# Performance work log

Hardware: AMD Instinct MI355X
Metric: run time of the kernel (lower is better)

## Reference

```python
import jax, jax.numpy as jnp
import numpy as np

T, L, D, P, H = 1024, 32, 512, 512, 2048
EPS = 1e-5  # torch LayerNorm default eps


def _layer_norm(x, g, b):
    m = x.mean(axis=-1, keepdims=True)
    v = ((x - m) ** 2).mean(axis=-1, keepdims=True)
    return (x - m) * jax.lax.rsqrt(v + EPS) * g + b


def setup_inputs() -> dict:
    key = jax.random.key(0)
    ks = jax.random.split(key, 16)
    s = 0.02
    inp = {
        "base_prompts": jax.random.normal(ks[0], (T, L, D), jnp.float32),
        "new_prompt": jax.random.normal(ks[1], (L, D), jnp.float32),
        "task_embedding": jax.random.normal(ks[2], (D,), jnp.float32),
        # linear weights stored (in, out) so forward is x @ W + b
        "Wt": jax.random.normal(ks[3], (D, P), jnp.float32) * s,
        "bt": jnp.zeros((P,), jnp.float32),
        "Wq": jax.random.normal(ks[4], (D, P), jnp.float32) * s,
        "bq": jnp.zeros((P,), jnp.float32),
        "Wk": jax.random.normal(ks[5], (D, P), jnp.float32) * s,
        "bk": jnp.zeros((P,), jnp.float32),
        "Wv": jax.random.normal(ks[6], (D, P), jnp.float32) * s,
        "bv": jnp.zeros((P,), jnp.float32),
        "Wo": jax.random.normal(ks[7], (P, D), jnp.float32) * s,
        "bo": jnp.zeros((D,), jnp.float32),
        "Wa1": jax.random.normal(ks[8], (D, H), jnp.float32) * s,
        "ba1": jnp.zeros((H,), jnp.float32),
        "Wa2": jax.random.normal(ks[9], (H, D), jnp.float32) * s,
        "ba2": jnp.zeros((D,), jnp.float32),
        "g_in": jnp.ones((D,), jnp.float32),
        "b_in": jnp.zeros((D,), jnp.float32),
        "g_out": jnp.ones((D,), jnp.float32),
        "b_out": jnp.zeros((D,), jnp.float32),
    }
    return inp


def reference(base_prompts, new_prompt, task_embedding,
              Wt, bt, Wq, bq, Wk, bk, Wv, bv, Wo, bo,
              Wa1, ba1, Wa2, ba2, g_in, b_in, g_out, b_out):
    scale = 1.0 / np.sqrt(P).astype(np.float32)

    # --- task conditioning ---
    task_vec = jnp.tanh(task_embedding @ Wt + bt)                 # [P]
    key_repr = (base_prompts @ Wk + bk).mean(axis=1)              # [T,P]
    scores = (key_repr @ task_vec) * scale                        # [T]
    task_weights = jax.nn.softmax(scores)
    conditioned = base_prompts * (1.0 + task_weights[:, None, None])  # [T,L,D]

    query = new_prompt @ Wq + bq                                  # [L,P]
    keys = conditioned @ Wk + bk                                  # [T,L,P]
    values = conditioned @ Wv + bv                                # [T,L,P]

    # --- task-level attention ---
    pooled_q = query.mean(axis=0)                                 # [P]
    pooled_k = keys.mean(axis=1)                                  # [T,P]
    task_attn = jax.nn.softmax((pooled_k @ pooled_q) * scale)     # [T]
    task_weights = 0.5 * task_weights + 0.5 * task_attn
    task_weights = task_weights / jnp.maximum(task_weights.sum(), 1e-6)

    # --- enhanced mode: weighted pooling over tasks ---
    weighted_values = jnp.einsum('t,tlp->lp', task_weights, values)       # [L,P]
    weighted_keys = jnp.einsum('t,tlp->lp', task_weights, keys)           # [L,P]
    weighted_prompts = jnp.einsum('t,tld->ld', task_weights, conditioned) # [L,D]

    # --- feature-level attention ---
    feature_logits = (query @ weighted_keys.T) * scale            # [L,L]
    feature_attn = jax.nn.softmax(feature_logits, axis=-1)
    evolved_proj = feature_attn @ weighted_values                 # [L,P]

    evolved = evolved_proj @ Wo + bo                              # [L,D]
    evolved = _layer_norm(weighted_prompts + evolved, g_in, b_in)
    mlp = jax.nn.relu(evolved @ Wa1 + ba1) @ Wa2 + ba2
    aligned = _layer_norm(evolved + mlp, g_out, b_out)            # [L,D]

    aligned_prompts = jnp.broadcast_to(aligned, (T, L, D))        # stack of identical aligned prompts
    return aligned, aligned_prompts, task_weights, feature_attn
```

## Files before the change

### kernel.cpp

```cpp
#include <hip/hip_runtime.h>


typedef unsigned int u32;

static constexpr int T_ = 1024, L_ = 32, D_ = 512, P_ = 512, H_ = 2048;
static constexpr float SCALE = 0.04419417382415922f;
static constexpr float EPS_ = 1e-5f;

static constexpr int OFF_QUERY   = 0;
static constexpr int OFF_TV      = 16384;
static constexpr int OFF_PQ      = 16896;
static constexpr int OFF_WKTV    = 17408;
static constexpr int OFF_WKPQ    = 17920;
static constexpr int OFF_U       = 18432;
static constexpr int OFF_V       = 19456;
static constexpr int OFF_C       = 20480;
static constexpr int OFF_PART    = 21504;
static constexpr int OFF_WBASE   = 545792;
static constexpr int OFF_WKEY    = 562176;
static constexpr int OFF_WVAL    = 578560;
static constexpr int OFF_FA      = 594944;
static constexpr int OFF_EP      = 595968;
static constexpr int OFF_EVOLVED = 612352;
static constexpr int OFF_AQ      = 628736;
static constexpr int OFF_AKV     = 645632;
static constexpr int OFF_AEVO    = 678400;
static constexpr int OFF_AH1     = 694784;
static constexpr int OFF_AOUT    = 760320;
static constexpr int ZERO_BEGIN  = OFF_AQ;
static constexpr int ZERO_F4     = (776704 - 628736) / 4;

static constexpr int OFFO_AL = 0;
static constexpr int OFFO_AP = 16384;
static constexpr int OFFO_TW = 16384 + 16777216;
static constexpr int OFFO_FA = OFFO_TW + 1024;

__device__ __forceinline__ float wred(float v) {
    #pragma unroll
    for (int off = 32; off > 0; off >>= 1) v += __shfl_down(v, off, 64);
    return v;
}
template <int NT>
__device__ __forceinline__ float fsum(float v, float* buf, int tid) {
    v = wred(v);
    if ((tid & 63) == 0) buf[tid >> 6] = v;
    __syncthreads();
    if (tid == 0) { float s = 0.f; for (int i = 0; i < NT / 64; ++i) s += buf[i]; buf[0] = s; }
    __syncthreads();
    float r = buf[0]; __syncthreads();
    return r;
}
template <int NT>
__device__ __forceinline__ float fmaxr(float v, float* buf, int tid) {
    #pragma unroll
    for (int off = 32; off > 0; off >>= 1) v = fmaxf(v, __shfl_down(v, off, 64));
    if ((tid & 63) == 0) buf[tid >> 6] = v;
    __syncthreads();
    if (tid == 0) { float s = buf[0]; for (int i = 1; i < NT / 64; ++i) s = fmaxf(s, buf[i]); buf[0] = s; }
    __syncthreads();
    float r = buf[0]; __syncthreads();
    return r;
}

__global__ void k_zero(float* __restrict__ ws) {
    int i = blockIdx.x * 256 + threadIdx.x;
    if (i < ZERO_F4) ((float4*)(ws + ZERO_BEGIN))[i] = make_float4(0.f, 0.f, 0.f, 0.f);
}

__global__ void k_query_g(const float* __restrict__ np, const float* __restrict__ te,
                          const float* __restrict__ Wq, const float* __restrict__ Wt,
                          float* __restrict__ ws) {
    __shared__ float sx[128];
    int p = threadIdx.x, b = blockIdx.x, kc = blockIdx.y;
    const float* x = (b < L_) ? (np + b * D_) : te;
    if (p < 128) sx[p] = x[kc * 128 + p];
    __syncthreads();
    const float* W = (b < L_) ? Wq : Wt;
    float acc = 0.f;
    #pragma unroll 8
    for (int j = 0; j < 128; ++j) acc = fmaf(sx[j], W[(kc * 128 + j) * P_ + p], acc);
    atomicAdd(&ws[OFF_AQ + b * P_ + p], acc);
}

__global__ void k_query_ep(const float* __restrict__ bq, const float* __restrict__ bt,
                           float* __restrict__ ws) {
    int p = threadIdx.x, b = blockIdx.x;
    if (b < L_) ws[OFF_QUERY + b * P_ + p] = ws[OFF_AQ + b * P_ + p] + bq[p];
    else        ws[OFF_TV + p] = tanhf(ws[OFF_AQ + L_ * P_ + p] + bt[p]);
}

__global__ void k_pq(float* __restrict__ ws) {
    int p = threadIdx.x;
    float s = 0.f;
    for (int l = 0; l < L_; ++l) s += ws[OFF_QUERY + l * P_ + p];
    ws[OFF_PQ + p] = s * (1.0f / L_);
}

__global__ void k_wk2(const float* __restrict__ Wk, float* __restrict__ ws) {
    int tid = threadIdx.x, wv = tid >> 6, lane = tid & 63;
    int d = blockIdx.x * 8 + wv;
    const float4* row = (const float4*)(Wk + d * P_);
    const float4* tv4 = (const float4*)(ws + OFF_TV);
    const float4* pq4 = (const float4*)(ws + OFF_PQ);
    float4 a = row[lane * 2], b = row[lane * 2 + 1];
    float4 t0 = tv4[lane * 2], t1 = tv4[lane * 2 + 1];
    float4 q0 = pq4[lane * 2], q1 = pq4[lane * 2 + 1];
    float pa = a.x * t0.x + a.y * t0.y + a.z * t0.z + a.w * t0.w
             + b.x * t1.x + b.y * t1.y + b.z * t1.z + b.w * t1.w;
    float pb = a.x * q0.x + a.y * q0.y + a.z * q0.z + a.w * q0.w
             + b.x * q1.x + b.y * q1.y + b.z * q1.z + b.w * q1.w;
    pa = wred(pa); pb = wred(pb);
    if (lane == 0) { ws[OFF_WKTV + d] = pa; ws[OFF_WKPQ + d] = pb; }
}

__global__ void k_bbar(const float* __restrict__ base, float* __restrict__ ws) {
    __shared__ float buf[8];
    int t = blockIdx.x, d = threadIdx.x;
    const float* bp = base + (size_t)t * (L_ * D_);
    float s = 0.f;
    for (int l = 0; l < L_; ++l) s += bp[l * D_ + d];
    float up = fsum<512>(s * ws[OFF_WKTV + d], buf, d);
    float vp = fsum<512>(s * ws[OFF_WKPQ + d], buf, d);
    if (d == 0) {
        ws[OFF_U + t] = up * (1.0f / L_);
        ws[OFF_V + t] = vp * (1.0f / L_);
    }
}

__global__ void k_soft(const float* __restrict__ bk, float* __restrict__ out_tw,
                       float* __restrict__ ws) {
    __shared__ float buf[8];
    int tid = threadIdx.x;
    float pbt = 0.f, pbq = 0.f;
    for (int p = tid; p < P_; p += 256) {
        float bkf = bk[p];
        pbt = fmaf(bkf, ws[OFF_TV + p], pbt);
        pbq = fmaf(bkf, ws[OFF_PQ + p], pbq);
    }
    float bkt = fsum<256>(pbt, buf, tid);
    float bkq = fsum<256>(pbq, buf, tid);

    float s1[4], e1[4], tw1[4], lmax = -1e30f;
    #pragma unroll
    for (int k = 0; k < 4; ++k) {
        s1[k] = (ws[OFF_U + tid + k * 256] + bkt) * SCALE;
        lmax = fmaxf(lmax, s1[k]);
    }
    float gmax = fmaxr<256>(lmax, buf, tid);
    float ls = 0.f;
    #pragma unroll
    for (int k = 0; k < 4; ++k) { e1[k] = expf(s1[k] - gmax); ls += e1[k]; }
    float gs = fsum<256>(ls, buf, tid);
    #pragma unroll
    for (int k = 0; k < 4; ++k) tw1[k] = e1[k] / gs;

    float p2[4], e2[4];
    lmax = -1e30f;
    #pragma unroll
    for (int k = 0; k < 4; ++k) {
        p2[k] = ((1.0f + tw1[k]) * ws[OFF_V + tid + k * 256] + bkq) * SCALE;
        lmax = fmaxf(lmax, p2[k]);
    }
    gmax = fmaxr<256>(lmax, buf, tid);
    ls = 0.f;
    #pragma unroll
    for (int k = 0; k < 4; ++k) { e2[k] = expf(p2[k] - gmax); ls += e2[k]; }
    gs = fsum<256>(ls, buf, tid);

    float tw[4], lsum = 0.f;
    #pragma unroll
    for (int k = 0; k < 4; ++k) { tw[k] = 0.5f * tw1[k] + 0.5f * (e2[k] / gs); lsum += tw[k]; }
    float S = fsum<256>(lsum, buf, tid);
    S = fmaxf(S, 1e-6f);
    #pragma unroll
    for (int k = 0; k < 4; ++k) {
        int t = tid + k * 256;
        float twn = tw[k] / S;
        out_tw[t] = twn;
        ws[OFF_C + t] = twn * (1.0f + tw1[k]);
    }
}

__global__ void k_wpart(const float* __restrict__ base, float* __restrict__ ws) {
    __shared__ float cs[32];
    int l = blockIdx.x, ch = blockIdx.y, tid = threadIdx.x;
    if (tid < 32) cs[tid] = ws[OFF_C + ch * 32 + tid];
    __syncthreads();
    float a0 = 0.f, a1 = 0.f, a2 = 0.f, a3 = 0.f;
    for (int i = 0; i < 32; ++i) {
        int t = ch * 32 + i;
        float4 v = ((const float4*)(base + ((size_t)t * L_ + l) * D_))[tid];
        float cc = cs[i];
        a0 = fmaf(cc, v.x, a0); a1 = fmaf(cc, v.y, a1);
        a2 = fmaf(cc, v.z, a2); a3 = fmaf(cc, v.w, a3);
    }
    ((float4*)(ws + OFF_PART + (ch * L_ + l) * D_))[tid] = make_float4(a0, a1, a2, a3);
}

__global__ void k_wred(float* __restrict__ ws) {
    int l = blockIdx.x, d = threadIdx.x;
    float s = 0.f;
    for (int ch = 0; ch < 32; ++ch) s += ws[OFF_PART + (ch * L_ + l) * D_ + d];
    ws[OFF_WBASE + l * D_ + d] = s;
}

__global__ void k_wkv_g(const float* __restrict__ Wk, const float* __restrict__ Wv,
                        float* __restrict__ ws) {
    __shared__ float sx[128];
    int p = threadIdx.x, l = blockIdx.x, sel = blockIdx.y, kc = blockIdx.z;
    if (p < 128) sx[p] = ws[OFF_WBASE + l * D_ + kc * 128 + p];
    __syncthreads();
    const float* W = sel ? Wv : Wk;
    float acc = 0.f;
    #pragma unroll 8
    for (int j = 0; j < 128; ++j) acc = fmaf(sx[j], W[(kc * 128 + j) * P_ + p], acc);
    atomicAdd(&ws[OFF_AKV + (sel * L_ + l) * P_ + p], acc);
}

__global__ void k_wkv_ep(const float* __restrict__ bk, const float* __restrict__ bv,
                         float* __restrict__ ws) {
    int p = threadIdx.x, l = blockIdx.x, sel = blockIdx.y;
    float b = sel ? bv[p] : bk[p];
    ws[(sel ? OFF_WVAL : OFF_WKEY) + l * P_ + p] = ws[OFF_AKV + (sel * L_ + l) * P_ + p] + b;
}

__global__ void k_logits(float* __restrict__ out_fa, float* __restrict__ ws) {
    __shared__ __align__(16) float sq[512];
    __shared__ float lg[32];
    int l = blockIdx.x, tid = threadIdx.x, wv = tid >> 6, lane = tid & 63;
    sq[tid] = ws[OFF_QUERY + l * P_ + tid];
    __syncthreads();
    const float4* sq4 = (const float4*)sq;
    float4 q0 = sq4[lane * 2], q1 = sq4[lane * 2 + 1];
    for (int g = wv * 4; g < wv * 4 + 4; ++g) {
        const float4* kr = (const float4*)(ws + OFF_WKEY + g * P_);
        float4 a = kr[lane * 2], b = kr[lane * 2 + 1];
        float s = a.x * q0.x + a.y * q0.y + a.z * q0.z + a.w * q0.w
                + b.x * q1.x + b.y * q1.y + b.z * q1.z + b.w * q1.w;
        s = wred(s);
        if (lane == 0) lg[g] = s * SCALE;
    }
    __syncthreads();
    if (tid < 32) {
        float mx = -1e30f;
        for (int i = 0; i < 32; ++i) mx = fmaxf(mx, lg[i]);
        float S = 0.f;
        for (int i = 0; i < 32; ++i) S += expf(lg[i] - mx);
        float f = expf(lg[tid] - mx) / S;
        ws[OFF_FA + l * 32 + tid] = f;
        out_fa[l * 32 + tid] = f;
    }
}

__global__ void k_ep(float* __restrict__ ws) {
    __shared__ float fa[32];
    int l = blockIdx.x, p = threadIdx.x;
    if (p < 32) fa[p] = ws[OFF_FA + l * 32 + p];
    __syncthreads();
    float acc = 0.f;
    #pragma unroll 8
    for (int j = 0; j < L_; ++j) acc = fmaf(fa[j], ws[OFF_WVAL + j * P_ + p], acc);
    ws[OFF_EP + l * P_ + p] = acc;
}

__global__ void k_evo_g(const float* __restrict__ Wo, float* __restrict__ ws) {
    __shared__ float sx[128];
    int d = threadIdx.x, l = blockIdx.x, kc = blockIdx.y;
    if (d < 128) sx[d] = ws[OFF_EP + l * P_ + kc * 128 + d];
    __syncthreads();
    float acc = 0.f;
    #pragma unroll 8
    for (int j = 0; j < 128; ++j) acc = fmaf(sx[j], Wo[(kc * 128 + j) * D_ + d], acc);
    atomicAdd(&ws[OFF_AEVO + l * D_ + d], acc);
}

__global__ void k_xin_ln(const float* __restrict__ bo, const float* __restrict__ g_in,
                         const float* __restrict__ b_in, float* __restrict__ ws) {
    __shared__ float buf[8];
    int l = blockIdx.x, d = threadIdx.x;
    float x = ws[OFF_WBASE + l * D_ + d] + ws[OFF_AEVO + l * D_ + d] + bo[d];
    float mean = fsum<512>(x, buf, d) * (1.0f / D_);
    float dx = x - mean;
    float var = fsum<512>(dx * dx, buf, d) * (1.0f / D_);
    ws[OFF_EVOLVED + l * D_ + d] = dx * rsqrtf(var + EPS_) * g_in[d] + b_in[d];
}

__global__ void k_mlp1_g(const float* __restrict__ Wa1, float* __restrict__ ws) {
    __shared__ float sx[128];
    int tid = threadIdx.x, l = blockIdx.x, hc = blockIdx.y, kc = blockIdx.z;
    if (tid < 128) sx[tid] = ws[OFF_EVOLVED + l * D_ + kc * 128 + tid];
    __syncthreads();
    int h = hc * 512 + tid;
    float acc = 0.f;
    #pragma unroll 8
    for (int j = 0; j < 128; ++j) acc = fmaf(sx[j], Wa1[(kc * 128 + j) * H_ + h], acc);
    atomicAdd(&ws[OFF_AH1 + l * H_ + h], acc);
}

__global__ void k_mlp2_g(const float* __restrict__ Wa2, const float* __restrict__ ba1,
                         float* __restrict__ ws) {
    __shared__ float sh[128];
    int d = threadIdx.x, l = blockIdx.x, kc = blockIdx.y;
    if (d < 128) {
        int h = kc * 128 + d;
        sh[d] = fmaxf(ws[OFF_AH1 + l * H_ + h] + ba1[h], 0.f);
    }
    __syncthreads();
    float acc = 0.f;
    #pragma unroll 8
    for (int j = 0; j < 128; ++j) acc = fmaf(sh[j], Wa2[(kc * 128 + j) * D_ + d], acc);
    atomicAdd(&ws[OFF_AOUT + l * D_ + d], acc);
}

__global__ void k_lnout(const float* __restrict__ ba2, const float* __restrict__ g_out,
                        const float* __restrict__ b_out, float* __restrict__ out_al,
                        float* __restrict__ ws) {
    __shared__ float buf[8];
    int l = blockIdx.x, d = threadIdx.x;
    float x = ws[OFF_EVOLVED + l * D_ + d] + ws[OFF_AOUT + l * D_ + d] + ba2[d];
    float mean = fsum<512>(x, buf, d) * (1.0f / D_);
    float dx = x - mean;
    float var = fsum<512>(dx * dx, buf, d) * (1.0f / D_);
    out_al[l * D_ + d] = dx * rsqrtf(var + EPS_) * g_out[d] + b_out[d];
}

__global__ void k_bcast(float* __restrict__ out) {
    const float4* src = (const float4*)out;
    float4* dst = (float4*)(out + OFFO_AP);
    int idx = blockIdx.x * 256 + threadIdx.x;
    #pragma unroll
    for (int k = 0; k < 4; ++k) {
        int v = idx + k * 1048576;
        dst[v] = src[v & 4095];
    }
}

extern "C" void kernel_launch(void* const* d_in, const int* in_sizes, int n_in,
                              void* d_out, int out_size, void* d_ws, size_t ws_size,
                              hipStream_t stream) {
    const float* base = (const float*)d_in[0];
    const float* np   = (const float*)d_in[1];
    const float* te   = (const float*)d_in[2];
    const float* Wt   = (const float*)d_in[3];
    const float* bt   = (const float*)d_in[4];
    const float* Wq   = (const float*)d_in[5];
    const float* bq   = (const float*)d_in[6];
    const float* Wk   = (const float*)d_in[7];
    const float* bk   = (const float*)d_in[8];
    const float* Wv   = (const float*)d_in[9];
    const float* bv   = (const float*)d_in[10];
    const float* Wo   = (const float*)d_in[11];
    const float* bo   = (const float*)d_in[12];
    const float* Wa1  = (const float*)d_in[13];
    const float* ba1  = (const float*)d_in[14];
    const float* Wa2  = (const float*)d_in[15];
    const float* ba2  = (const float*)d_in[16];
    const float* g_in = (const float*)d_in[17];
    const float* b_in = (const float*)d_in[18];
    const float* g_out= (const float*)d_in[19];
    const float* b_out= (const float*)d_in[20];
    float* out = (float*)d_out;
    float* ws = out + OFFO_AP;

    hipLaunchKernelGGL(k_zero,     dim3(145),        dim3(256), 0, stream, ws);
    hipLaunchKernelGGL(k_query_g,  dim3(33, 4),      dim3(512), 0, stream, np, te, Wq, Wt, ws);
    hipLaunchKernelGGL(k_query_ep, dim3(33),         dim3(512), 0, stream, bq, bt, ws);
    hipLaunchKernelGGL(k_pq,       dim3(1),          dim3(512), 0, stream, ws);
    hipLaunchKernelGGL(k_wk2,      dim3(64),         dim3(512), 0, stream, Wk, ws);
    hipLaunchKernelGGL(k_bbar,     dim3(1024),       dim3(512), 0, stream, base, ws);
    hipLaunchKernelGGL(k_soft,     dim3(1),          dim3(256), 0, stream, bk, out + OFFO_TW, ws);
    hipLaunchKernelGGL(k_wpart,    dim3(32, 32),     dim3(128), 0, stream, base, ws);
    hipLaunchKernelGGL(k_wred,     dim3(32),         dim3(512), 0, stream, ws);
    hipLaunchKernelGGL(k_wkv_g,    dim3(32, 2, 4),   dim3(512), 0, stream, Wk, Wv, ws);
    hipLaunchKernelGGL(k_wkv_ep,   dim3(32, 2),      dim3(512), 0, stream, bk, bv, ws);
    hipLaunchKernelGGL(k_logits,   dim3(32),         dim3(512), 0, stream, out + OFFO_FA, ws);
    hipLaunchKernelGGL(k_ep,       dim3(32),         dim3(512), 0, stream, ws);
    hipLaunchKernelGGL(k_evo_g,    dim3(32, 4),      dim3(512), 0, stream, Wo, ws);
    hipLaunchKernelGGL(k_xin_ln,   dim3(32),         dim3(512), 0, stream, bo, g_in, b_in, ws);
    hipLaunchKernelGGL(k_mlp1_g,   dim3(32, 4, 4),   dim3(512), 0, stream, Wa1, ws);
    hipLaunchKernelGGL(k_mlp2_g,   dim3(32, 16),     dim3(512), 0, stream, Wa2, ba1, ws);
    hipLaunchKernelGGL(k_lnout,    dim3(32),         dim3(512), 0, stream, ba2, g_out, b_out, out + OFFO_AL, ws);
    hipLaunchKernelGGL(k_bcast,    dim3(4096),       dim3(256), 0, stream, out);
}
```

Before: 254.6 us.

## Fuse all stages into one cooperative persistent kernel with grid syncs

Replaces the chain of nineteen small kernel launches with a single cooperative kernel of 256 blocks that steps through the stages separated by grid-wide barriers. The L-sum of base_prompts is computed once and stored, and the split-K atomic GEMV stages are replaced by full-K per-block dot products or partial buffers, which removes the zeroing kernel and the atomics. The intent is to cut launch overhead and inter-kernel gaps. In exchange, most stages leave the majority of blocks idle at each barrier, and every grid sync adds its own latency.

Result: slower. 600.6 us (+135.9%).

```diff
diff --git a/kernel.cpp b/kernel.cpp
--- a/kernel.cpp
+++ b/kernel.cpp
@@ -1,4 +1,7 @@
 #include <hip/hip_runtime.h>
+#include <hip/hip_cooperative_groups.h>
+
+namespace cg = cooperative_groups;
 
 
 typedef unsigned int u32;
@@ -15,370 +18,339 @@
 static constexpr int OFF_U       = 18432;
 static constexpr int OFF_V       = 19456;
 static constexpr int OFF_C       = 20480;
-static constexpr int OFF_PART    = 21504;
-static constexpr int OFF_WBASE   = 545792;
-static constexpr int OFF_WKEY    = 562176;
-static constexpr int OFF_WVAL    = 578560;
-static constexpr int OFF_FA      = 594944;
-static constexpr int OFF_EP      = 595968;
-static constexpr int OFF_EVOLVED = 612352;
-static constexpr int OFF_AQ      = 628736;
-static constexpr int OFF_AKV     = 645632;
-static constexpr int OFF_AEVO    = 678400;
-static constexpr int OFF_AH1     = 694784;
-static constexpr int OFF_AOUT    = 760320;
-static constexpr int ZERO_BEGIN  = OFF_AQ;
-static constexpr int ZERO_F4     = (776704 - 628736) / 4;
+static constexpr int OFF_SBUF    = 21504;
+static constexpr int OFF_PART    = 545792;
+static constexpr int OFF_WBASE   = 676864;
+static constexpr int OFF_WKEY    = 693248;
+static constexpr int OFF_WVAL    = 709632;
+static constexpr int OFF_FA      = 726016;
+static constexpr int OFF_EVOLVED = 727040;
+static constexpr int OFF_H1      = 743424;
+static constexpr int OFF_P2      = 808960;
 
 static constexpr int OFFO_AL = 0;
 static constexpr int OFFO_AP = 16384;
 static constexpr int OFFO_TW = 16384 + 16777216;
 static constexpr int OFFO_FA = OFFO_TW + 1024;
 
+struct Params {
+    const float *base, *np, *te, *Wt, *bt, *Wq, *bq, *Wk, *bk, *Wv, *bv,
+                *Wo, *bo, *Wa1, *ba1, *Wa2, *ba2, *g_in, *b_in, *g_out, *b_out;
+    float* out;
+};
+
 __device__ __forceinline__ float wred(float v) {
     #pragma unroll
     for (int off = 32; off > 0; off >>= 1) v += __shfl_down(v, off, 64);
     return v;
 }
-template <int NT>
-__device__ __forceinline__ float fsum(float v, float* buf, int tid) {
+__device__ __forceinline__ float fsum512(float v, float* buf, int tid) {
     v = wred(v);
     if ((tid & 63) == 0) buf[tid >> 6] = v;
     __syncthreads();
-    if (tid == 0) { float s = 0.f; for (int i = 0; i < NT / 64; ++i) s += buf[i]; buf[0] = s; }
-    __syncthreads();
-    float r = buf[0]; __syncthreads();
+    if (tid == 0) { float s = 0.f; for (int i = 0; i < 8; ++i) s += buf[i]; buf[0] = s; }
+    __syncthreads();
+    float r = buf[0];
+    __syncthreads();
     return r;
 }
-template <int NT>
-__device__ __forceinline__ float fmaxr(float v, float* buf, int tid) {
+__device__ __forceinline__ float fmax512(float v, float* buf, int tid) {
     #pragma unroll
     for (int off = 32; off > 0; off >>= 1) v = fmaxf(v, __shfl_down(v, off, 64));
     if ((tid & 63) == 0) buf[tid >> 6] = v;
     __syncthreads();
-    if (tid == 0) { float s = buf[0]; for (int i = 1; i < NT / 64; ++i) s = fmaxf(s, buf[i]); buf[0] = s; }
-    __syncthreads();
-    float r = buf[0]; __syncthreads();
+    if (tid == 0) { float s = buf[0]; for (int i = 1; i < 8; ++i) s = fmaxf(s, buf[i]); buf[0] = s; }
+    __syncthreads();
+    float r = buf[0];
+    __syncthreads();
     return r;
 }
 
-__global__ void k_zero(float* __restrict__ ws) {
-    int i = blockIdx.x * 256 + threadIdx.x;
-    if (i < ZERO_F4) ((float4*)(ws + ZERO_BEGIN))[i] = make_float4(0.f, 0.f, 0.f, 0.f);
-}
-
-__global__ void k_query_g(const float* __restrict__ np, const float* __restrict__ te,
-                          const float* __restrict__ Wq, const float* __restrict__ Wt,
-                          float* __restrict__ ws) {
-    __shared__ float sx[128];
-    int p = threadIdx.x, b = blockIdx.x, kc = blockIdx.y;
-    const float* x = (b < L_) ? (np + b * D_) : te;
-    if (p < 128) sx[p] = x[kc * 128 + p];
-    __syncthreads();
-    const float* W = (b < L_) ? Wq : Wt;
-    float acc = 0.f;
-    #pragma unroll 8
-    for (int j = 0; j < 128; ++j) acc = fmaf(sx[j], W[(kc * 128 + j) * P_ + p], acc);
-    atomicAdd(&ws[OFF_AQ + b * P_ + p], acc);
-}
-
-__global__ void k_query_ep(const float* __restrict__ bq, const float* __restrict__ bt,
-                           float* __restrict__ ws) {
-    int p = threadIdx.x, b = blockIdx.x;
-    if (b < L_) ws[OFF_QUERY + b * P_ + p] = ws[OFF_AQ + b * P_ + p] + bq[p];
-    else        ws[OFF_TV + p] = tanhf(ws[OFF_AQ + L_ * P_ + p] + bt[p]);
-}
-
-__global__ void k_pq(float* __restrict__ ws) {
-    int p = threadIdx.x;
-    float s = 0.f;
-    for (int l = 0; l < L_; ++l) s += ws[OFF_QUERY + l * P_ + p];
-    ws[OFF_PQ + p] = s * (1.0f / L_);
-}
-
-__global__ void k_wk2(const float* __restrict__ Wk, float* __restrict__ ws) {
-    int tid = threadIdx.x, wv = tid >> 6, lane = tid & 63;
-    int d = blockIdx.x * 8 + wv;
-    const float4* row = (const float4*)(Wk + d * P_);
-    const float4* tv4 = (const float4*)(ws + OFF_TV);
-    const float4* pq4 = (const float4*)(ws + OFF_PQ);
-    float4 a = row[lane * 2], b = row[lane * 2 + 1];
-    float4 t0 = tv4[lane * 2], t1 = tv4[lane * 2 + 1];
-    float4 q0 = pq4[lane * 2], q1 = pq4[lane * 2 + 1];
-    float pa = a.x * t0.x + a.y * t0.y + a.z * t0.z + a.w * t0.w
-             + b.x * t1.x + b.y * t1.y + b.z * t1.z + b.w * t1.w;
-    float pb = a.x * q0.x + a.y * q0.y + a.z * q0.z + a.w * q0.w
-             + b.x * q1.x + b.y * q1.y + b.z * q1.z + b.w * q1.w;
-    pa = wred(pa); pb = wred(pb);
-    if (lane == 0) { ws[OFF_WKTV + d] = pa; ws[OFF_WKPQ + d] = pb; }
-}
-
-__global__ void k_bbar(const float* __restrict__ base, float* __restrict__ ws) {
+__global__ void __launch_bounds__(512) k_mega(Params P) {
+    cg::grid_group g = cg::this_grid();
+    __shared__ __align__(16) float sm[576];
     __shared__ float buf[8];
-    int t = blockIdx.x, d = threadIdx.x;
-    const float* bp = base + (size_t)t * (L_ * D_);
-    float s = 0.f;
-    for (int l = 0; l < L_; ++l) s += bp[l * D_ + d];
-    float up = fsum<512>(s * ws[OFF_WKTV + d], buf, d);
-    float vp = fsum<512>(s * ws[OFF_WKPQ + d], buf, d);
-    if (d == 0) {
-        ws[OFF_U + t] = up * (1.0f / L_);
-        ws[OFF_V + t] = vp * (1.0f / L_);
-    }
-}
-
-__global__ void k_soft(const float* __restrict__ bk, float* __restrict__ out_tw,
-                       float* __restrict__ ws) {
-    __shared__ float buf[8];
-    int tid = threadIdx.x;
-    float pbt = 0.f, pbq = 0.f;
-    for (int p = tid; p < P_; p += 256) {
-        float bkf = bk[p];
-        pbt = fmaf(bkf, ws[OFF_TV + p], pbt);
-        pbq = fmaf(bkf, ws[OFF_PQ + p], pbq);
-    }
-    float bkt = fsum<256>(pbt, buf, tid);
-    float bkq = fsum<256>(pbq, buf, tid);
-
-    float s1[4], e1[4], tw1[4], lmax = -1e30f;
-    #pragma unroll
-    for (int k = 0; k < 4; ++k) {
-        s1[k] = (ws[OFF_U + tid + k * 256] + bkt) * SCALE;
-        lmax = fmaxf(lmax, s1[k]);
-    }
-    float gmax = fmaxr<256>(lmax, buf, tid);
-    float ls = 0.f;
-    #pragma unroll
-    for (int k = 0; k < 4; ++k) { e1[k] = expf(s1[k] - gmax); ls += e1[k]; }
-    float gs = fsum<256>(ls, buf, tid);
-    #pragma unroll
-    for (int k = 0; k < 4; ++k) tw1[k] = e1[k] / gs;
-
-    float p2[4], e2[4];
-    lmax = -1e30f;
-    #pragma unroll
-    for (int k = 0; k < 4; ++k) {
-        p2[k] = ((1.0f + tw1[k]) * ws[OFF_V + tid + k * 256] + bkq) * SCALE;
-        lmax = fmaxf(lmax, p2[k]);
-    }
-    gmax = fmaxr<256>(lmax, buf, tid);
-    ls = 0.f;
-    #pragma unroll
-    for (int k = 0; k < 4; ++k) { e2[k] = expf(p2[k] - gmax); ls += e2[k]; }
-    gs = fsum<256>(ls, buf, tid);
-
-    float tw[4], lsum = 0.f;
-    #pragma unroll
-    for (int k = 0; k < 4; ++k) { tw[k] = 0.5f * tw1[k] + 0.5f * (e2[k] / gs); lsum += tw[k]; }
-    float S = fsum<256>(lsum, buf, tid);
-    S = fmaxf(S, 1e-6f);
-    #pragma unroll
-    for (int k = 0; k < 4; ++k) {
-        int t = tid + k * 256;
-        float twn = tw[k] / S;
-        out_tw[t] = twn;
-        ws[OFF_C + t] = twn * (1.0f + tw1[k]);
-    }
-}
-
-__global__ void k_wpart(const float* __restrict__ base, float* __restrict__ ws) {
-    __shared__ float cs[32];
-    int l = blockIdx.x, ch = blockIdx.y, tid = threadIdx.x;
-    if (tid < 32) cs[tid] = ws[OFF_C + ch * 32 + tid];
-    __syncthreads();
-    float a0 = 0.f, a1 = 0.f, a2 = 0.f, a3 = 0.f;
-    for (int i = 0; i < 32; ++i) {
-        int t = ch * 32 + i;
-        float4 v = ((const float4*)(base + ((size_t)t * L_ + l) * D_))[tid];
-        float cc = cs[i];
-        a0 = fmaf(cc, v.x, a0); a1 = fmaf(cc, v.y, a1);
-        a2 = fmaf(cc, v.z, a2); a3 = fmaf(cc, v.w, a3);
-    }
-    ((float4*)(ws + OFF_PART + (ch * L_ + l) * D_))[tid] = make_float4(a0, a1, a2, a3);
-}
-
-__global__ void k_wred(float* __restrict__ ws) {
-    int l = blockIdx.x, d = threadIdx.x;
-    float s = 0.f;
-    for (int ch = 0; ch < 32; ++ch) s += ws[OFF_PART + (ch * L_ + l) * D_ + d];
-    ws[OFF_WBASE + l * D_ + d] = s;
-}
-
-__global__ void k_wkv_g(const float* __restrict__ Wk, const float* __restrict__ Wv,
-                        float* __restrict__ ws) {
-    __shared__ float sx[128];
-    int p = threadIdx.x, l = blockIdx.x, sel = blockIdx.y, kc = blockIdx.z;
-    if (p < 128) sx[p] = ws[OFF_WBASE + l * D_ + kc * 128 + p];
-    __syncthreads();
-    const float* W = sel ? Wv : Wk;
-    float acc = 0.f;
-    #pragma unroll 8
-    for (int j = 0; j < 128; ++j) acc = fmaf(sx[j], W[(kc * 128 + j) * P_ + p], acc);
-    atomicAdd(&ws[OFF_AKV + (sel * L_ + l) * P_ + p], acc);
-}
-
-__global__ void k_wkv_ep(const float* __restrict__ bk, const float* __restrict__ bv,
-                         float* __restrict__ ws) {
-    int p = threadIdx.x, l = blockIdx.x, sel = blockIdx.y;
-    float b = sel ? bv[p] : bk[p];
-    ws[(sel ? OFF_WVAL : OFF_WKEY) + l * P_ + p] = ws[OFF_AKV + (sel * L_ + l) * P_ + p] + b;
-}
-
-__global__ void k_logits(float* __restrict__ out_fa, float* __restrict__ ws) {
-    __shared__ __align__(16) float sq[512];
-    __shared__ float lg[32];
-    int l = blockIdx.x, tid = threadIdx.x, wv = tid >> 6, lane = tid & 63;
-    sq[tid] = ws[OFF_QUERY + l * P_ + tid];
-    __syncthreads();
-    const float4* sq4 = (const float4*)sq;
-    float4 q0 = sq4[lane * 2], q1 = sq4[lane * 2 + 1];
-    for (int g = wv * 4; g < wv * 4 + 4; ++g) {
-        const float4* kr = (const float4*)(ws + OFF_WKEY + g * P_);
-        float4 a = kr[lane * 2], b = kr[lane * 2 + 1];
-        float s = a.x * q0.x + a.y * q0.y + a.z * q0.z + a.w * q0.w
-                + b.x * q1.x + b.y * q1.y + b.z * q1.z + b.w * q1.w;
-        s = wred(s);
-        if (lane == 0) lg[g] = s * SCALE;
-    }
-    __syncthreads();
-    if (tid < 32) {
-        float mx = -1e30f;
-        for (int i = 0; i < 32; ++i) mx = fmaxf(mx, lg[i]);
-        float S = 0.f;
-        for (int i = 0; i < 32; ++i) S += expf(lg[i] - mx);
-        float f = expf(lg[tid] - mx) / S;
-        ws[OFF_FA + l * 32 + tid] = f;
-        out_fa[l * 32 + tid] = f;
-    }
-}
-
-__global__ void k_ep(float* __restrict__ ws) {
-    __shared__ float fa[32];
-    int l = blockIdx.x, p = threadIdx.x;
-    if (p < 32) fa[p] = ws[OFF_FA + l * 32 + p];
-    __syncthreads();
-    float acc = 0.f;
-    #pragma unroll 8
-    for (int j = 0; j < L_; ++j) acc = fmaf(fa[j], ws[OFF_WVAL + j * P_ + p], acc);
-    ws[OFF_EP + l * P_ + p] = acc;
-}
-
-__global__ void k_evo_g(const float* __restrict__ Wo, float* __restrict__ ws) {
-    __shared__ float sx[128];
-    int d = threadIdx.x, l = blockIdx.x, kc = blockIdx.y;
-    if (d < 128) sx[d] = ws[OFF_EP + l * P_ + kc * 128 + d];
-    __syncthreads();
-    float acc = 0.f;
-    #pragma unroll 8
-    for (int j = 0; j < 128; ++j) acc = fmaf(sx[j], Wo[(kc * 128 + j) * D_ + d], acc);
-    atomicAdd(&ws[OFF_AEVO + l * D_ + d], acc);
-}
-
-__global__ void k_xin_ln(const float* __restrict__ bo, const float* __restrict__ g_in,
-                         const float* __restrict__ b_in, float* __restrict__ ws) {
-    __shared__ float buf[8];
-    int l = blockIdx.x, d = threadIdx.x;
-    float x = ws[OFF_WBASE + l * D_ + d] + ws[OFF_AEVO + l * D_ + d] + bo[d];
-    float mean = fsum<512>(x, buf, d) * (1.0f / D_);
-    float dx = x - mean;
-    float var = fsum<512>(dx * dx, buf, d) * (1.0f / D_);
-    ws[OFF_EVOLVED + l * D_ + d] = dx * rsqrtf(var + EPS_) * g_in[d] + b_in[d];
-}
-
-__global__ void k_mlp1_g(const float* __restrict__ Wa1, float* __restrict__ ws) {
-    __shared__ float sx[128];
-    int tid = threadIdx.x, l = blockIdx.x, hc = blockIdx.y, kc = blockIdx.z;
-    if (tid < 128) sx[tid] = ws[OFF_EVOLVED + l * D_ + kc * 128 + tid];
-    __syncthreads();
-    int h = hc * 512 + tid;
-    float acc = 0.f;
-    #pragma unroll 8
-    for (int j = 0; j < 128; ++j) acc = fmaf(sx[j], Wa1[(kc * 128 + j) * H_ + h], acc);
-    atomicAdd(&ws[OFF_AH1 + l * H_ + h], acc);
-}
-
-__global__ void k_mlp2_g(const float* __restrict__ Wa2, const float* __restrict__ ba1,
-                         float* __restrict__ ws) {
-    __shared__ float sh[128];
-    int d = threadIdx.x, l = blockIdx.x, kc = blockIdx.y;
-    if (d < 128) {
-        int h = kc * 128 + d;
-        sh[d] = fmaxf(ws[OFF_AH1 + l * H_ + h] + ba1[h], 0.f);
-    }
-    __syncthreads();
-    float acc = 0.f;
-    #pragma unroll 8
-    for (int j = 0; j < 128; ++j) acc = fmaf(sh[j], Wa2[(kc * 128 + j) * D_ + d], acc);
-    atomicAdd(&ws[OFF_AOUT + l * D_ + d], acc);
-}
-
-__global__ void k_lnout(const float* __restrict__ ba2, const float* __restrict__ g_out,
-                        const float* __restrict__ b_out, float* __restrict__ out_al,
-                        float* __restrict__ ws) {
-    __shared__ float buf[8];
-    int l = blockIdx.x, d = threadIdx.x;
-    float x = ws[OFF_EVOLVED + l * D_ + d] + ws[OFF_AOUT + l * D_ + d] + ba2[d];
-    float mean = fsum<512>(x, buf, d) * (1.0f / D_);
-    float dx = x - mean;
-    float var = fsum<512>(dx * dx, buf, d) * (1.0f / D_);
-    out_al[l * D_ + d] = dx * rsqrtf(var + EPS_) * g_out[d] + b_out[d];
-}
-
-__global__ void k_bcast(float* __restrict__ out) {
-    const float4* src = (const float4*)out;
-    float4* dst = (float4*)(out + OFFO_AP);
-    int idx = blockIdx.x * 256 + threadIdx.x;
-    #pragma unroll
-    for (int k = 0; k < 4; ++k) {
-        int v = idx + k * 1048576;
-        dst[v] = src[v & 4095];
+    const int b = blockIdx.x, tid = threadIdx.x;
+    float* out = P.out;
+    float* ws = out + OFFO_AP;
+
+    for (int i = 0; i < 4; ++i) {
+        int t = b + i * 256;
+        const float* bp = P.base + (size_t)t * (L_ * D_) + tid;
+        float s = 0.f;
+        #pragma unroll
+        for (int l = 0; l < L_; ++l) s += bp[l * D_];
+        ws[OFF_SBUF + t * D_ + tid] = s;
+    }
+    if (b < 33) {
+        const float* x = (b < L_) ? (P.np + b * D_) : P.te;
+        const float* W = (b < L_) ? P.Wq : P.Wt;
+        sm[tid] = x[tid];
+        __syncthreads();
+        float a0 = 0, a1 = 0, a2 = 0, a3 = 0;
+        for (int d = 0; d < D_; d += 4) {
+            a0 = fmaf(sm[d],     W[(size_t)(d)     * P_ + tid], a0);
+            a1 = fmaf(sm[d + 1], W[(size_t)(d + 1) * P_ + tid], a1);
+            a2 = fmaf(sm[d + 2], W[(size_t)(d + 2) * P_ + tid], a2);
+            a3 = fmaf(sm[d + 3], W[(size_t)(d + 3) * P_ + tid], a3);
+        }
+        float acc = (a0 + a1) + (a2 + a3);
+        if (b < L_) ws[OFF_QUERY + b * P_ + tid] = acc + P.bq[tid];
+        else        ws[OFF_TV + tid] = tanhf(acc + P.bt[tid]);
+    }
+    g.sync();
+
+    if (b < 64) {
+        float s = 0.f;
+        #pragma unroll
+        for (int l = 0; l < L_; ++l) s += ws[OFF_QUERY + l * P_ + tid];
+        s *= (1.0f / L_);
+        sm[tid] = s;
+        if (b == 0) ws[OFF_PQ + tid] = s;
+        __syncthreads();
+        int wv = tid >> 6, lane = tid & 63;
+        int d = b * 8 + wv;
+        const float4* row = (const float4*)(P.Wk + (size_t)d * P_);
+        const float4* tv4 = (const float4*)(ws + OFF_TV);
+        const float4* pq4 = (const float4*)sm;
+        float4 a = row[lane * 2], c = row[lane * 2 + 1];
+        float4 t0 = tv4[lane * 2], t1 = tv4[lane * 2 + 1];
+        float4 q0 = pq4[lane * 2], q1 = pq4[lane * 2 + 1];
+        float pa = a.x * t0.x + a.y * t0.y + a.z * t0.z + a.w * t0.w
+                 + c.x * t1.x + c.y * t1.y + c.z * t1.z + c.w * t1.w;
+        float pb = a.x * q0.x + a.y * q0.y + a.z * q0.z + a.w * q0.w
+                 + c.x * q1.x + c.y * q1.y + c.z * q1.z + c.w * q1.w;
+        pa = wred(pa); pb = wred(pb);
+        if (lane == 0) { ws[OFF_WKTV + d] = pa; ws[OFF_WKPQ + d] = pb; }
+    }
+    g.sync();
+
+    {
+        float wt = ws[OFF_WKTV + tid], wq = ws[OFF_WKPQ + tid];
+        for (int i = 0; i < 4; ++i) {
+            int t = b * 4 + i;
+            float s = ws[OFF_SBUF + t * D_ + tid];
+            float up = fsum512(s * wt, buf, tid);
+            float vp = fsum512(s * wq, buf, tid);
+            if (tid == 0) {
+                ws[OFF_U + t] = up * (1.0f / L_);
+                ws[OFF_V + t] = vp * (1.0f / L_);
+            }
+        }
+    }
+    g.sync();
+
+    if (b == 0) {
+        float bkt = fsum512(P.bk[tid] * ws[OFF_TV + tid], buf, tid);
+        float bkq = fsum512(P.bk[tid] * ws[OFF_PQ + tid], buf, tid);
+
+        float s1[2], e1[2], tw1[2], lmax = -1e30f;
+        #pragma unroll
+        for (int k = 0; k < 2; ++k) {
+            s1[k] = (ws[OFF_U + tid + k * 512] + bkt) * SCALE;
+            lmax = fmaxf(lmax, s1[k]);
+        }
+        float gmax = fmax512(lmax, buf, tid);
+        float ls = 0.f;
+        #pragma unroll
+        for (int k = 0; k < 2; ++k) { e1[k] = expf(s1[k] - gmax); ls += e1[k]; }
+        float gs = fsum512(ls, buf, tid);
+        #pragma unroll
+        for (int k = 0; k < 2; ++k) tw1[k] = e1[k] / gs;
+
+        float p2[2], e2[2];
+        lmax = -1e30f;
+        #pragma unroll
+        for (int k = 0; k < 2; ++k) {
+            p2[k] = ((1.0f + tw1[k]) * ws[OFF_V + tid + k * 512] + bkq) * SCALE;
+            lmax = fmaxf(lmax, p2[k]);
+        }
+        gmax = fmax512(lmax, buf, tid);
+        ls = 0.f;
+        #pragma unroll
+        for (int k = 0; k < 2; ++k) { e2[k] = expf(p2[k] - gmax); ls += e2[k]; }
+        gs = fsum512(ls, buf, tid);
+
+        float tw[2], lsum = 0.f;
+        #pragma unroll
+        for (int k = 0; k < 2; ++k) { tw[k] = 0.5f * tw1[k] + 0.5f * (e2[k] / gs); lsum += tw[k]; }
+        float S = fsum512(lsum, buf, tid);
+        S = fmaxf(S, 1e-6f);
+        #pragma unroll
+        for (int k = 0; k < 2; ++k) {
+            int t = tid + k * 512;
+            float twn = tw[k] / S;
+            out[OFFO_TW + t] = twn;
+            ws[OFF_C + t] = twn * (1.0f + tw1[k]);
+        }
+    }
+    g.sync();
+
+    {
+        int l = b >> 3, tc = b & 7;
+        if (tid < 128) sm[tid] = ws[OFF_C + tc * 128 + tid];
+        __syncthreads();
+        const float* bp = P.base + ((size_t)(tc * 128) * L_ + l) * D_ + tid;
+        float acc = 0.f;
+        for (int i = 0; i < 128; ++i)
+            acc = fmaf(sm[i], bp[(size_t)i * (L_ * D_)], acc);
+        ws[OFF_PART + (l * 8 + tc) * D_ + tid] = acc;
+    }
+    g.sync();
+
+    if (b < 64) {
+        int l = b >> 1, sel = b & 1;
+        float wsum = 0.f;
+        #pragma unroll
+        for (int tc = 0; tc < 8; ++tc) wsum += ws[OFF_PART + (l * 8 + tc) * D_ + tid];
+        sm[tid] = wsum;
+        if (sel == 0) ws[OFF_WBASE + l * D_ + tid] = wsum;
+        __syncthreads();
+        const float* W = sel ? P.Wv : P.Wk;
+        float a0 = 0, a1 = 0, a2 = 0, a3 = 0;
+        for (int d = 0; d < D_; d += 4) {
+            a0 = fmaf(sm[d],     W[(size_t)(d)     * P_ + tid], a0);
+            a1 = fmaf(sm[d + 1], W[(size_t)(d + 1) * P_ + tid], a1);
+            a2 = fmaf(sm[d + 2], W[(size_t)(d + 2) * P_ + tid], a2);
+            a3 = fmaf(sm[d + 3], W[(size_t)(d + 3) * P_ + tid], a3);
+        }
+        float acc = (a0 + a1) + (a2 + a3) + (sel ? P.bv[tid] : P.bk[tid]);
+        ws[(sel ? OFF_WVAL : OFF_WKEY) + l * P_ + tid] = acc;
+    }
+    g.sync();
+
+    if (b < 32) {
+        sm[tid] = ws[OFF_QUERY + b * P_ + tid];
+        __syncthreads();
+        int wv = tid >> 6, lane = tid & 63;
+        const float4* sq4 = (const float4*)sm;
+        float4 q0 = sq4[lane * 2], q1 = sq4[lane * 2 + 1];
+        for (int gg = wv * 4; gg < wv * 4 + 4; ++gg) {
+            const float4* kr = (const float4*)(ws + OFF_WKEY + (size_t)gg * P_);
+            float4 a = kr[lane * 2], c = kr[lane * 2 + 1];
+            float s = a.x * q0.x + a.y * q0.y + a.z * q0.z + a.w * q0.w
+                    + c.x * q1.x + c.y * q1.y + c.z * q1.z + c.w * q1.w;
+            s = wred(s);
+            if (lane == 0) sm[512 + gg] = s * SCALE;
+        }
+        __syncthreads();
+        if (tid < 32) {
+            float mx = -1e30f;
+            for (int i = 0; i < 32; ++i) mx = fmaxf(mx, sm[512 + i]);
+            float S = 0.f;
+            for (int i = 0; i < 32; ++i) S += expf(sm[512 + i] - mx);
+            float f = expf(sm[512 + tid] - mx) / S;
+            ws[OFF_FA + b * 32 + tid] = f;
+            out[OFFO_FA + b * 32 + tid] = f;
+        }
+    }
+    g.sync();
+
+    if (b < 32) {
+        if (tid < 32) sm[512 + tid] = ws[OFF_FA + b * 32 + tid];
+        __syncthreads();
+        float ep = 0.f;
+        #pragma unroll
+        for (int j = 0; j < 32; ++j) ep = fmaf(sm[512 + j], ws[OFF_WVAL + j * P_ + tid], ep);
+        __syncthreads();
+        sm[tid] = ep;
+        __syncthreads();
+        float a0 = 0, a1 = 0, a2 = 0, a3 = 0;
+        for (int p = 0; p < P_; p += 4) {
+            a0 = fmaf(sm[p],     P.Wo[(size_t)(p)     * D_ + tid], a0);
+            a1 = fmaf(sm[p + 1], P.Wo[(size_t)(p + 1) * D_ + tid], a1);
+            a2 = fmaf(sm[p + 2], P.Wo[(size_t)(p + 2) * D_ + tid], a2);
+            a3 = fmaf(sm[p + 3], P.Wo[(size_t)(p + 3) * D_ + tid], a3);
+        }
+        float x = ws[OFF_WBASE + b * D_ + tid] + (a0 + a1) + (a2 + a3) + P.bo[tid];
+        float mean = fsum512(x, buf, tid) * (1.0f / D_);
+        float dx = x - mean;
+        float var = fsum512(dx * dx, buf, tid) * (1.0f / D_);
+        ws[OFF_EVOLVED + b * D_ + tid] = dx * rsqrtf(var + EPS_) * P.g_in[tid] + P.b_in[tid];
+    }
+    g.sync();
+
+    if (b < 128) {
+        int l = b >> 2, hc = b & 3;
+        sm[tid] = ws[OFF_EVOLVED + l * D_ + tid];
+        __syncthreads();
+        int h = hc * 512 + tid;
+        float a0 = 0, a1 = 0, a2 = 0, a3 = 0;
+        for (int d = 0; d < D_; d += 4) {
+            a0 = fmaf(sm[d],     P.Wa1[(size_t)(d)     * H_ + h], a0);
+            a1 = fmaf(sm[d + 1], P.Wa1[(size_t)(d + 1) * H_ + h], a1);
+            a2 = fmaf(sm[d + 2], P.Wa1[(size_t)(d + 2) * H_ + h], a2);
+            a3 = fmaf(sm[d + 3], P.Wa1[(size_t)(d + 3) * H_ + h], a3);
+        }
+        ws[OFF_H1 + l * H_ + h] = fmaxf((a0 + a1) + (a2 + a3) + P.ba1[h], 0.f);
+    }
+    g.sync();
+
+    {
+        int l = b >> 3, kc = b & 7;
+        if (tid < 256) sm[tid] = ws[OFF_H1 + l * H_ + kc * 256 + tid];
+        __syncthreads();
+        float a0 = 0, a1 = 0, a2 = 0, a3 = 0;
+        for (int j = 0; j < 256; j += 4) {
+            a0 = fmaf(sm[j],     P.Wa2[(size_t)(kc * 256 + j)     * D_ + tid], a0);
+            a1 = fmaf(sm[j + 1], P.Wa2[(size_t)(kc * 256 + j + 1) * D_ + tid], a1);
+            a2 = fmaf(sm[j + 2], P.Wa2[(size_t)(kc * 256 + j + 2) * D_ + tid], a2);
+            a3 = fmaf(sm[j + 3], P.Wa2[(size_t)(kc * 256 + j + 3) * D_ + tid], a3);
+        }
+        ws[OFF_P2 + (l * 8 + kc) * D_ + tid] = (a0 + a1) + (a2 + a3);
+    }
+    g.sync();
+
+    if (b < 32) {
+        float x = ws[OFF_EVOLVED + b * D_ + tid] + P.ba2[tid];
+        #pragma unroll
+        for (int kc = 0; kc < 8; ++kc) x += ws[OFF_P2 + (b * 8 + kc) * D_ + tid];
+        float mean = fsum512(x, buf, tid) * (1.0f / D_);
+        float dx = x - mean;
+        float var = fsum512(dx * dx, buf, tid) * (1.0f / D_);
+        out[OFFO_AL + b * D_ + tid] = dx * rsqrtf(var + EPS_) * P.g_out[tid] + P.b_out[tid];
+    }
+    g.sync();
+
+    {
+        const float4* src = (const float4*)out;
+        float4* dst = (float4*)(out + OFFO_AP);
+        int gt = b * 512 + tid;
+        #pragma unroll
+        for (int k = 0; k < 32; ++k) {
+            int v = gt + k * 131072;
+            dst[v] = src[v & 4095];
+        }
     }
 }
 
 extern "C" void kernel_launch(void* const* d_in, const int* in_sizes, int n_in,
                               void* d_out, int out_size, void* d_ws, size_t ws_size,
                               hipStream_t stream) {
-    const float* base = (const float*)d_in[0];
-    const float* np   = (const float*)d_in[1];
-    const float* te   = (const float*)d_in[2];
-    const float* Wt   = (const float*)d_in[3];
-    const float* bt   = (const float*)d_in[4];
-    const float* Wq   = (const float*)d_in[5];
-    const float* bq   = (const float*)d_in[6];
-    const float* Wk   = (const float*)d_in[7];
-    const float* bk   = (const float*)d_in[8];
-    const float* Wv   = (const float*)d_in[9];
-    const float* bv   = (const float*)d_in[10];
-    const float* Wo   = (const float*)d_in[11];
-    const float* bo   = (const float*)d_in[12];
-    const float* Wa1  = (const float*)d_in[13];
-    const float* ba1  = (const float*)d_in[14];
-    const float* Wa2  = (const float*)d_in[15];
-    const float* ba2  = (const float*)d_in[16];
-    const float* g_in = (const float*)d_in[17];
-    const float* b_in = (const float*)d_in[18];
-    const float* g_out= (const float*)d_in[19];
-    const float* b_out= (const float*)d_in[20];
-    float* out = (float*)d_out;
-    float* ws = out + OFFO_AP;
-
-    hipLaunchKernelGGL(k_zero,     dim3(145),        dim3(256), 0, stream, ws);
-    hipLaunchKernelGGL(k_query_g,  dim3(33, 4),      dim3(512), 0, stream, np, te, Wq, Wt, ws);
-    hipLaunchKernelGGL(k_query_ep, dim3(33),         dim3(512), 0, stream, bq, bt, ws);
-    hipLaunchKernelGGL(k_pq,       dim3(1),          dim3(512), 0, stream, ws);
-    hipLaunchKernelGGL(k_wk2,      dim3(64),         dim3(512), 0, stream, Wk, ws);
-    hipLaunchKernelGGL(k_bbar,     dim3(1024),       dim3(512), 0, stream, base, ws);
-    hipLaunchKernelGGL(k_soft,     dim3(1),          dim3(256), 0, stream, bk, out + OFFO_TW, ws);
-    hipLaunchKernelGGL(k_wpart,    dim3(32, 32),     dim3(128), 0, stream, base, ws);
-    hipLaunchKernelGGL(k_wred,     dim3(32),         dim3(512), 0, stream, ws);
-    hipLaunchKernelGGL(k_wkv_g,    dim3(32, 2, 4),   dim3(512), 0, stream, Wk, Wv, ws);
-    hipLaunchKernelGGL(k_wkv_ep,   dim3(32, 2),      dim3(512), 0, stream, bk, bv, ws);
-    hipLaunchKernelGGL(k_logits,   dim3(32),         dim3(512), 0, stream, out + OFFO_FA, ws);
-    hipLaunchKernelGGL(k_ep,       dim3(32),         dim3(512), 0, stream, ws);
-    hipLaunchKernelGGL(k_evo_g,    dim3(32, 4),      dim3(512), 0, stream, Wo, ws);
-    hipLaunchKernelGGL(k_xin_ln,   dim3(32),         dim3(512), 0, stream, bo, g_in, b_in, ws);
-    hipLaunchKernelGGL(k_mlp1_g,   dim3(32, 4, 4),   dim3(512), 0, stream, Wa1, ws);
-    hipLaunchKernelGGL(k_mlp2_g,   dim3(32, 16),     dim3(512), 0, stream, Wa2, ba1, ws);
-    hipLaunchKernelGGL(k_lnout,    dim3(32),         dim3(512), 0, stream, ba2, g_out, b_out, out + OFFO_AL, ws);
-    hipLaunchKernelGGL(k_bcast,    dim3(4096),       dim3(256), 0, stream, out);
-}
+    Params Pm;
+    Pm.base = (const float*)d_in[0];
+    Pm.np   = (const float*)d_in[1];
+    Pm.te   = (const float*)d_in[2];
+    Pm.Wt   = (const float*)d_in[3];
+    Pm.bt   = (const float*)d_in[4];
+    Pm.Wq   = (const float*)d_in[5];
+    Pm.bq   = (const float*)d_in[6];
+    Pm.Wk   = (const float*)d_in[7];
+    Pm.bk   = (const float*)d_in[8];
+    Pm.Wv   = (const float*)d_in[9];
+    Pm.bv   = (const float*)d_in[10];
+    Pm.Wo   = (const float*)d_in[11];
+    Pm.bo   = (const float*)d_in[12];
+    Pm.Wa1  = (const float*)d_in[13];
+    Pm.ba1  = (const float*)d_in[14];
+    Pm.Wa2  = (const float*)d_in[15];
+    Pm.ba2  = (const float*)d_in[16];
+    Pm.g_in = (const float*)d_in[17];
+    Pm.b_in = (const float*)d_in[18];
+    Pm.g_out= (const float*)d_in[19];
+    Pm.b_out= (const float*)d_in[20];
+    Pm.out  = (float*)d_out;
+
+    void* args[] = { &Pm };
+    hipLaunchCooperativeKernel((const void*)k_mega, dim3(256), dim3(512), args, 0, stream);
+}
```
